# Optimization experiments

Measured on AMD Instinct MI355X. Metric: run time of the kernel, lower is better.

The kernel has to match this reference:

```python
import jax, jax.numpy as jnp
import numpy as np
import math

NHEADS = 4


def _mab(Q, K, qw, qb, kw, kb, vw, vb, ow, ob, mask):
    """MAB2 from tripletformer: multi-head attention (head split via cat(split,0)),
    softmax scale uses sqrt(FULL dim_V), masked_fill(mask==0, -1e10), residual on
    the projected Q, then O + relu(fc_o(O))."""
    dv = qw.shape[1]
    dh = dv // NHEADS
    B, Nq, _ = Q.shape
    Nk = K.shape[1]
    Qh = (Q @ qw + qb).reshape(B, Nq, NHEADS, dh).transpose(0, 2, 1, 3)  # B,h,Nq,dh
    Kh = (K @ kw + kb).reshape(B, Nk, NHEADS, dh).transpose(0, 2, 1, 3)
    Vh = (K @ vw + vb).reshape(B, Nk, NHEADS, dh).transpose(0, 2, 1, 3)
    att = jnp.einsum('bhqd,bhkd->bhqk', Qh, Kh) * (1.0 / math.sqrt(dv))
    att = jnp.where(mask, att, jnp.asarray(-1e10, att.dtype))
    A = jax.nn.softmax(att, axis=-1)
    Oh = Qh + jnp.einsum('bhqk,bhkd->bhqd', A, Vh)
    O = Oh.transpose(0, 2, 1, 3).reshape(B, Nq, dv)
    return O + jax.nn.relu(O @ ow + ob)


def _forward(context_x, value, mask, obs_len, iff_w, iff_b, ind_points,
             q0w, q0b, k0w, k0b, v0w, v0b, o0w, o0b,
             q1w, q1b, k1w, k1b, v1w, v1b, o1w, o1b):
    B, L = context_x.shape
    D = value.shape[-1]
    mflat = mask.reshape(B, L * D)
    # stable stream compaction: observed entries first, original (time-major,
    # channel-minor) order preserved; truncate to static obs_len
    order = jnp.argsort(-mflat, axis=-1, stable=True)[:, :obs_len]  # (B, N)
    T = jnp.broadcast_to(context_x[:, :, None], (B, L, D)).reshape(B, L * D)
    C = jnp.broadcast_to(jnp.arange(D, dtype=jnp.int32), (B, L, D)).reshape(B, L * D)
    U = value.reshape(B, L * D)
    take = lambda a: jnp.take_along_axis(a, order, axis=-1)
    T_, U_, mk_ = take(T), take(U), take(mflat)
    Ch = jax.nn.one_hot(take(C), D, dtype=value.dtype)  # one_hot(num_classes=dim-2)
    X = jnp.concatenate([Ch, T_[..., None], U_[..., None]], axis=-1) * mk_[..., None]
    Y = jax.nn.relu(X @ iff_w + iff_b) * mk_[..., None]
    key_valid = mk_ > 0                        # (B, N)
    mask1 = key_valid[:, None, None, :]        # mab0: mask padded keys
    mask2 = key_valid[:, None, :, None]        # mab1: mask padded query rows
    Z = Y
    n_layers = ind_points.shape[0]
    for i in range(n_layers):
        I = jnp.broadcast_to(ind_points[i], (B,) + ind_points[i].shape)
        H = _mab(I, Z, q0w[i], q0b[i], k0w[i], k0b[i], v0w[i], v0b[i], o0w[i], o0b[i], mask1)
        Zn = _mab(Z, H, q1w[i], q1b[i], k1w[i], k1b[i], v1w[i], v1b[i], o1w[i], o1b[i], mask2)
        Z = Zn * mk_[..., None] + Z
    return Z, mk_[..., None]


def setup_inputs() -> dict:
    B, L, D, OBS, DK, M, NL = 16, 512, 41, 4096, 128, 128, 3
    key = jax.random.key(0)
    ks = jax.random.split(key, 16)
    context_x = jnp.sort(jax.random.uniform(ks[0], (B, L), dtype=jnp.float32), axis=-1)
    value = jax.random.normal(ks[1], (B, L, D), dtype=jnp.float32)
    # exactly OBS observed entries per batch row -> static packed length
    r = jax.random.uniform(ks[2], (B, L * D))
    kth = jnp.sort(r, axis=-1)[:, OBS]
    mask = (r < kth[:, None]).astype(jnp.float32).reshape(B, L, D)

    def w(k, shape, fan):
        return jax.random.normal(k, shape, dtype=jnp.float32) / math.sqrt(fan)

    inp = dict(
        context_x=context_x, value=value, mask=mask, obs_len=OBS,
        iff_w=w(ks[3], (D + 2, DK), D + 2), iff_b=jnp.zeros((DK,), jnp.float32),
        ind_points=w(ks[4], (NL, M, DK), DK),
    )
    for j, n in enumerate(['q0', 'k0', 'v0', 'o0', 'q1', 'k1', 'v1', 'o1']):
        inp[n + 'w'] = w(ks[5 + j], (NL, DK, DK), DK)
        inp[n + 'b'] = jnp.zeros((NL, DK), jnp.float32)
    return inp


def reference(context_x, value, mask, obs_len, iff_w, iff_b, ind_points,
              q0w, q0b, k0w, k0b, v0w, v0b, o0w, o0b,
              q1w, q1b, k1w, k1b, v1w, v1b, o1w, o1b):
    return _forward(context_x, value, mask, obs_len, iff_w, iff_b, ind_points,
                    q0w, q0b, k0w, k0b, v0w, v0b, o0w, o0b,
                    q1w, q1b, k1w, k1b, v1w, v1b, o1w, o1b)
```

## Files before the change

### kernel.cpp

```cpp
#include <hip/hip_runtime.h>
#include <math.h>

#define NBATCH 16
#define SEQL   512
#define DIM    41
#define LDFLAT (SEQL*DIM)
#define OBS    4096
#define DK     128
#define NH     4
#define DH     32

typedef short bf16x8 __attribute__((ext_vector_type(8)));
typedef short short8v __attribute__((ext_vector_type(8)));
typedef float floatx4 __attribute__((ext_vector_type(4)));

__device__ __forceinline__ short f2bf(float f) {
  union { float f; unsigned u; } v;
  v.f = f;
  unsigned r = (v.u + 0x7fffu + ((v.u >> 16) & 1u)) >> 16;
  return (short)r;
}
__device__ __forceinline__ float bf2f(short s) {
  union { unsigned u; float f; } v;
  v.u = ((unsigned)(unsigned short)s) << 16;
  return v.f;
}

__device__ __forceinline__ void stage_w(short* Wl, const short* __restrict__ Wt,
                                        int tid) {
#pragma unroll
  for (int i = tid * 8; i < 128 * 128; i += 2048)
    *(int4*)&Wl[(i >> 7) * 136 + (i & 127)] = *(const int4*)&Wt[i];
}
__device__ __forceinline__ void load_af(const short* Xl, int wv, int lm,
                                        int quad, bf16x8 af[4]) {
#pragma unroll
  for (int kc = 0; kc < 4; kc++)
    af[kc] = *(bf16x8*)&Xl[(wv * 16 + lm) * 136 + kc * 32 + quad * 8];
}
__device__ __forceinline__ void gemm8(const short* Wl, const bf16x8 af[4],
                                      int lm, int quad, floatx4 acc[8]) {
#pragma unroll
  for (int nt = 0; nt < 8; nt++) acc[nt] = (floatx4){0.f, 0.f, 0.f, 0.f};
#pragma unroll
  for (int kc = 0; kc < 4; kc++) {
    bf16x8 a = af[kc];
#pragma unroll
    for (int nt = 0; nt < 8; nt++) {
      bf16x8 b = *(bf16x8*)&Wl[(nt * 16 + lm) * 136 + kc * 32 + quad * 8];
      acc[nt] = __builtin_amdgcn_mfma_f32_16x16x32_bf16(a, b, acc[nt], 0, 0, 0);
    }
  }
}
__device__ __forceinline__ void store_sl(short* Sl, const floatx4 acc[8],
                                         const float* __restrict__ bias,
                                         int wv, int lm, int quad) {
#pragma unroll
  for (int nt = 0; nt < 8; nt++) {
    int col = nt * 16 + lm;
    float bn = bias[col];
#pragma unroll
    for (int r = 0; r < 4; r++)
      Sl[(wv * 16 + quad * 4 + r) * 136 + col] = f2bf(acc[nt][r] + bn);
  }
}
__device__ __forceinline__ void write_hs(const short* Sl,
                                         short* __restrict__ out, int rb,
                                         int nshift, int tid) {
  int rr = tid >> 2, hh = tid & 3;
  int r = rb + rr;
  int bb = r >> nshift, nn = r & ((1 << nshift) - 1);
  size_t o = (((size_t)(bb * NH + hh) << nshift) + nn) * 32;
#pragma unroll
  for (int j = 0; j < 4; j++)
    *(int4*)&out[o + j * 8] = *(int4*)&Sl[rr * 136 + hh * 32 + j * 8];
}

__global__ __launch_bounds__(1024) void prep_build_kernel(
    const float* __restrict__ q0w, const float* __restrict__ k0w,
    const float* __restrict__ v0w, const float* __restrict__ o0w,
    const float* __restrict__ q1w, const float* __restrict__ k1w,
    const float* __restrict__ v1w, const float* __restrict__ o1w,
    short* __restrict__ Wt,
    const float* __restrict__ mask, int* __restrict__ order,
    float* __restrict__ mk_out, float* __restrict__ mk_out2) {
  __shared__ float Tl[128 * 132];
  __shared__ int wsums[16];
  __shared__ int s_total_ones;
  __shared__ int s_chunk_ones;
  __shared__ int s_ones_base;
  __shared__ int s_zeros_base;
  int tid = threadIdx.x;

  if (blockIdx.x < 24) {
    int id = blockIdx.x, l = id >> 3, wi = id & 7;
    const float* s;
    switch (wi) {
      case 0: s = q0w; break; case 1: s = k0w; break;
      case 2: s = v0w; break; case 3: s = o0w; break;
      case 4: s = q1w; break; case 5: s = k1w; break;
      case 6: s = v1w; break; default: s = o1w; break;
    }
    s += (size_t)l * 16384;
    for (int i = tid * 4; i < 16384; i += 4096) {
      int k = i >> 7, n = i & 127;
      float4 x = *(const float4*)&s[i];
      Tl[k * 132 + n + 0] = x.x; Tl[k * 132 + n + 1] = x.y;
      Tl[k * 132 + n + 2] = x.z; Tl[k * 132 + n + 3] = x.w;
    }
    __syncthreads();
    short* dst = Wt + (size_t)id * 16384;
    int n = tid >> 3, k0 = (tid & 7) * 16;
    for (int jc = 0; jc < 2; jc++) {
      short8v t;
#pragma unroll
      for (int j = 0; j < 8; j++) t[j] = f2bf(Tl[(k0 + jc * 8 + j) * 132 + n]);
      *(short8v*)&dst[n * 128 + k0 + jc * 8] = t;
    }
    return;
  }

  int b = blockIdx.x - 24;
  const float* m = mask + (size_t)b * LDFLAT;
  int lane = tid & 63, w = tid >> 6;

  int cnt = 0;
  for (int j = tid; j < LDFLAT; j += 1024) cnt += (m[j] > 0.f) ? 1 : 0;
  for (int off = 32; off > 0; off >>= 1) cnt += __shfl_xor(cnt, off);
  if (lane == 0) wsums[w] = cnt;
  __syncthreads();
  if (tid == 0) {
    int t = 0;
    for (int i = 0; i < 16; i++) t += wsums[i];
    s_total_ones = t; s_ones_base = 0; s_zeros_base = 0;
  }
  __syncthreads();
  int total_ones = s_total_ones;

  for (int c0 = 0; c0 < LDFLAT; c0 += 1024) {
    __syncthreads();
    int j = c0 + tid;
    bool valid = (j < LDFLAT);
    float mv = valid ? m[j] : 0.f;
    int one = (valid && mv > 0.f) ? 1 : 0;
    int v = one;
    for (int off = 1; off < 64; off <<= 1) {
      int t = __shfl_up(v, (unsigned)off);
      if (lane >= off) v += t;
    }
    if (lane == 63) wsums[w] = v;
    __syncthreads();
    if (tid == 0) {
      int run = 0;
      for (int i = 0; i < 16; i++) { int t = wsums[i]; wsums[i] = run; run += t; }
      s_chunk_ones = run;
    }
    __syncthreads();
    int ones_before = (v - one) + wsums[w];
    int ob = s_ones_base, zb = s_zeros_base, chunk_ones = s_chunk_ones;
    int rem = LDFLAT - c0;
    int chunk_valid = rem < 1024 ? rem : 1024;
    int valid_before = tid < rem ? tid : rem;
    if (valid) {
      int pos = one ? (ob + ones_before)
                    : (total_ones + zb + (valid_before - ones_before));
      if (pos < OBS) {
        order[b * OBS + pos] = j;
        mk_out[b * OBS + pos] = mv;
        mk_out2[b * OBS + pos] = mv;
      }
    }
    __syncthreads();
    if (tid == 0) {
      s_ones_base = ob + chunk_ones;
      s_zeros_base = zb + (chunk_valid - chunk_ones);
    }
  }
}

__global__ __launch_bounds__(256) void fusedA_kernel(
    const int* __restrict__ order, const float* __restrict__ mk_g,
    const float* __restrict__ cx, const float* __restrict__ value,
    const float* __restrict__ iff_w, const float* __restrict__ iff_b,
    float* __restrict__ Z,
    const short* __restrict__ Wk, const float* __restrict__ kbias,
    short* __restrict__ Kb,
    const short* __restrict__ Wv, const float* __restrict__ vbias,
    short* __restrict__ Vb,
    const short* __restrict__ Wq, const float* __restrict__ qbias,
    short* __restrict__ Qb,
    const float* __restrict__ indp, const short* __restrict__ WtAll,
    const float* __restrict__ q0b_all, short* __restrict__ qh_b) {
  __shared__ __align__(16) short Xl[64 * 136];
  __shared__ __align__(16) short Wl[128 * 136];
  __shared__ int   rdd[64];
  __shared__ float rdt[64], rdu[64], rdm[64];
  int tid = threadIdx.x;

  if (blockIdx.x >= 1024) {
    int id = blockIdx.x - 1024;
    int l = id >> 1, rbq = (id & 1) * 64;
    const float* X = indp + (size_t)l * 16384 + (size_t)rbq * 128;
    const short* W = WtAll + (size_t)(l * 8) * 16384;
    const float* bias = q0b_all + (size_t)l * 128;
    short* out = qh_b + (size_t)l * 16384;
    for (int i = tid * 4; i < 64 * 128; i += 1024) {
      int rr = i >> 7, c = i & 127;
      float4 x = *(const float4*)&X[i];
      *(short4*)&Xl[rr * 136 + c] =
          make_short4(f2bf(x.x), f2bf(x.y), f2bf(x.z), f2bf(x.w));
    }
    stage_w(Wl, W, tid);
    __syncthreads();
    int wv = tid >> 6, lane = tid & 63, lm = lane & 15, quad = lane >> 4;
    bf16x8 af[4];
    load_af(Xl, wv, lm, quad, af);
    floatx4 acc[8];
    gemm8(Wl, af, lm, quad, acc);
    __syncthreads();
    store_sl(Wl, acc, bias, wv, lm, quad);
    __syncthreads();
    write_hs(Wl, out, rbq, 7, tid);
    return;
  }

  int rb = blockIdx.x * 64;
  if (tid < 64) {
    int idx = rb + tid;
    int b = idx >> 12;
    int j = order[idx];
    int l = j / DIM;
    rdd[tid] = j - l * DIM;
    rdt[tid] = cx[b * SEQL + l];
    rdu[tid] = value[(size_t)b * LDFLAT + j];
    rdm[tid] = mk_g[idx];
  }
  stage_w(Wl, Wk, tid);
  __syncthreads();
  for (int i = tid; i < 64 * 128; i += 256) {
    int rr = i >> 7, k = i & 127;
    float y = iff_w[rdd[rr] * DK + k] + rdt[rr] * iff_w[41 * DK + k] +
              rdu[rr] * iff_w[42 * DK + k] + iff_b[k];
    float z = fmaxf(y, 0.f) * rdm[rr];
    Z[(size_t)(rb + rr) * DK + k] = z;
    Xl[rr * 136 + k] = f2bf(z);
  }
  __syncthreads();
  int wv = tid >> 6, lane = tid & 63, lm = lane & 15, quad = lane >> 4;
  bf16x8 af[4];
  load_af(Xl, wv, lm, quad, af);
  floatx4 acc[8];
  gemm8(Wl, af, lm, quad, acc);
  __syncthreads();
  store_sl(Wl, acc, kbias, wv, lm, quad);
  __syncthreads();
  write_hs(Wl, Kb, rb, 12, tid);
  __syncthreads();
  stage_w(Wl, Wv, tid);
  __syncthreads();
  gemm8(Wl, af, lm, quad, acc);
  __syncthreads();
  store_sl(Wl, acc, vbias, wv, lm, quad);
  __syncthreads();
  write_hs(Wl, Vb, rb, 12, tid);
  __syncthreads();
  stage_w(Wl, Wq, tid);
  __syncthreads();
  gemm8(Wl, af, lm, quad, acc);
  __syncthreads();
  store_sl(Wl, acc, qbias, wv, lm, quad);
  __syncthreads();
  write_hs(Wl, Qb, rb, 12, tid);
}

__global__ __launch_bounds__(256) void attn1_kernel(
    const short* __restrict__ Qh,
    const short* __restrict__ Kh, const short* __restrict__ Vh,
    const float* __restrict__ mk,
    float* __restrict__ Opart, float* __restrict__ mpart,
    float* __restrict__ lpart) {
  __shared__ __align__(16) short Ql[128 * 40];
  __shared__ __align__(16) short Kc[64 * 40];
  __shared__ __align__(16) short Vtc[32 * 72];
  __shared__ __align__(16) short Pl[128 * 72];
  __shared__ float mkc[64];
  int bh = blockIdx.x;
  int b = bh >> 2, h = bh & 3;
  int ks = blockIdx.y;
  int tid = threadIdx.x;
  int wv = tid >> 6, lane = tid & 63, lm = lane & 15, quad = lane >> 4;

  const short* qbg = Qh + (size_t)h * 128 * 32;
  for (int i = tid * 8; i < 128 * 32; i += 2048) {
    int r = i >> 5, c = i & 31;
    *(int4*)&Ql[r * 40 + c] = *(const int4*)&qbg[i];
  }
  __syncthreads();
  bf16x8 aq[2];
  aq[0] = *(bf16x8*)&Ql[(wv * 32 + lm) * 40 + quad * 8];
  aq[1] = *(bf16x8*)&Ql[(wv * 32 + 16 + lm) * 40 + quad * 8];

  float m_i[2][4], l_i[2][4];
  floatx4 oacc[2][2];
#pragma unroll
  for (int mt = 0; mt < 2; mt++) {
#pragma unroll
    for (int r = 0; r < 4; r++) { m_i[mt][r] = -1e30f; l_i[mt][r] = 0.f; }
    oacc[mt][0] = (floatx4){0.f, 0.f, 0.f, 0.f};
    oacc[mt][1] = (floatx4){0.f, 0.f, 0.f, 0.f};
  }
  const float scale = 0.08838834764831845f;
  const short* kbase = Kh + ((size_t)bh * OBS + ks * 512) * 32;
  const short* vbase = Vh + ((size_t)bh * OBS + ks * 512) * 32;
  const float* mkb = mk + (size_t)b * OBS + ks * 512;

  for (int ch = 0; ch < 8; ch++) {
    __syncthreads();
    {
      int i = tid * 8;
      int r = i >> 5, c = i & 31;
      *(int4*)&Kc[r * 40 + c] = *(const int4*)&kbase[ch * 2048 + i];
      int4 vv4 = *(const int4*)&vbase[ch * 2048 + i];
      short* vv = (short*)&vv4;
#pragma unroll
      for (int j = 0; j < 8; j++) Vtc[(c + j) * 72 + r] = vv[j];
    }
    if (tid < 64) mkc[tid] = mkb[ch * 64 + tid];
    __syncthreads();

    floatx4 sf[2][4];
#pragma unroll
    for (int nt = 0; nt < 4; nt++) {
      bf16x8 bfrag = *(bf16x8*)&Kc[(nt * 16 + lm) * 40 + quad * 8];
      floatx4 z = {0.f, 0.f, 0.f, 0.f};
      sf[0][nt] = __builtin_amdgcn_mfma_f32_16x16x32_bf16(aq[0], bfrag, z, 0, 0, 0);
      sf[1][nt] = __builtin_amdgcn_mfma_f32_16x16x32_bf16(aq[1], bfrag, z, 0, 0, 0);
    }
#pragma unroll
    for (int nt = 0; nt < 4; nt++) {
      float mkv = mkc[nt * 16 + lm];
      bool ok = mkv > 0.f;
#pragma unroll
      for (int mt = 0; mt < 2; mt++)
#pragma unroll
        for (int r = 0; r < 4; r++)
          sf[mt][nt][r] = ok ? sf[mt][nt][r] * scale : -1e10f;
    }
#pragma unroll
    for (int mt = 0; mt < 2; mt++) {
#pragma unroll
      for (int r = 0; r < 4; r++) {
        float mx = fmaxf(fmaxf(sf[mt][0][r], sf[mt][1][r]),
                         fmaxf(sf[mt][2][r], sf[mt][3][r]));
        mx = fmaxf(mx, __shfl_xor(mx, 1));
        mx = fmaxf(mx, __shfl_xor(mx, 2));
        mx = fmaxf(mx, __shfl_xor(mx, 4));
        mx = fmaxf(mx, __shfl_xor(mx, 8));
        float mn = fmaxf(m_i[mt][r], mx);
        float al = __expf(m_i[mt][r] - mn);
        float ps = 0.f;
#pragma unroll
        for (int nt = 0; nt < 4; nt++) {
          float p = __expf(sf[mt][nt][r] - mn);
          sf[mt][nt][r] = p;
          ps += p;
        }
        ps += __shfl_xor(ps, 1);
        ps += __shfl_xor(ps, 2);
        ps += __shfl_xor(ps, 4);
        ps += __shfl_xor(ps, 8);
        l_i[mt][r] = l_i[mt][r] * al + ps;
        m_i[mt][r] = mn;
        oacc[mt][0] *= al;
        oacc[mt][1] *= al;
      }
    }
#pragma unroll
    for (int mt = 0; mt < 2; mt++)
#pragma unroll
      for (int nt = 0; nt < 4; nt++)
#pragma unroll
        for (int r = 0; r < 4; r++)
          Pl[(wv * 32 + mt * 16 + quad * 4 + r) * 72 + nt * 16 + lm] =
              f2bf(sf[mt][nt][r]);
#pragma unroll
    for (int kc = 0; kc < 2; kc++) {
      bf16x8 vf0 = *(bf16x8*)&Vtc[lm * 72 + kc * 32 + quad * 8];
      bf16x8 vf1 = *(bf16x8*)&Vtc[(16 + lm) * 72 + kc * 32 + quad * 8];
#pragma unroll
      for (int mt = 0; mt < 2; mt++) {
        bf16x8 pf = *(bf16x8*)&Pl[(wv * 32 + mt * 16 + lm) * 72 + kc * 32 + quad * 8];
        oacc[mt][0] = __builtin_amdgcn_mfma_f32_16x16x32_bf16(pf, vf0, oacc[mt][0], 0, 0, 0);
        oacc[mt][1] = __builtin_amdgcn_mfma_f32_16x16x32_bf16(pf, vf1, oacc[mt][1], 0, 0, 0);
      }
    }
  }
  float* ob = Opart + (size_t)(ks * 64 + bh) * 128 * 32;
#pragma unroll
  for (int mt = 0; mt < 2; mt++) {
#pragma unroll
    for (int r = 0; r < 4; r++) {
      int row = wv * 32 + mt * 16 + quad * 4 + r;
      ob[(size_t)row * 32 + lm] = oacc[mt][0][r];
      ob[(size_t)row * 32 + 16 + lm] = oacc[mt][1][r];
      if (lm == 0) {
        mpart[(size_t)(ks * 64 + bh) * 128 + row] = m_i[mt][r];
        lpart[(size_t)(ks * 64 + bh) * 128 + row] = l_i[mt][r];
      }
    }
  }
}

__global__ __launch_bounds__(256) void fusedB_kernel(
    const float* __restrict__ Opart, const float* __restrict__ mpart,
    const float* __restrict__ lpart, const short* __restrict__ qh,
    const short* __restrict__ Wo, const float* __restrict__ obias,
    const short* __restrict__ Wk, const float* __restrict__ kbias,
    const short* __restrict__ Wv, const float* __restrict__ vbias,
    short* __restrict__ khb, short* __restrict__ vhb) {
  __shared__ __align__(16) short Xl[64 * 136];
  __shared__ __align__(16) short Wl[128 * 136];
  int tid = threadIdx.x;
  int rb = blockIdx.x * 64;
  int b = rb >> 7, n0 = rb & 127;
  {
    int rr = tid >> 2, hh = tid & 3;
    int n = n0 + rr;
    int bh = b * 4 + hh;
    float mv[8], lv[8], m = -1e30f;
#pragma unroll
    for (int s = 0; s < 8; s++) {
      mv[s] = mpart[(size_t)(s * 64 + bh) * 128 + n];
      lv[s] = lpart[(size_t)(s * 64 + bh) * 128 + n];
      m = fmaxf(m, mv[s]);
    }
    float l = 0.f;
    float oa[32];
#pragma unroll
    for (int d = 0; d < 32; d++) oa[d] = 0.f;
#pragma unroll
    for (int s = 0; s < 8; s++) {
      float w = __expf(mv[s] - m);
      l += lv[s] * w;
      const float* op = &Opart[((size_t)(s * 64 + bh) * 128 + n) * 32];
#pragma unroll
      for (int d4 = 0; d4 < 8; d4++) {
        float4 v = *(const float4*)&op[d4 * 4];
        oa[d4 * 4 + 0] += v.x * w; oa[d4 * 4 + 1] += v.y * w;
        oa[d4 * 4 + 2] += v.z * w; oa[d4 * 4 + 3] += v.w * w;
      }
    }
    float li = 1.f / l;
    const short* qp = &qh[((size_t)hh * 128 + n) * 32];
#pragma unroll
    for (int d = 0; d < 32; d++)
      Xl[rr * 136 + hh * 32 + d] = f2bf(bf2f(qp[d]) + oa[d] * li);
  }
  stage_w(Wl, Wo, tid);
  __syncthreads();
  int wv = tid >> 6, lane = tid & 63, lm = lane & 15, quad = lane >> 4;
  bf16x8 af[4];
  load_af(Xl, wv, lm, quad, af);
  floatx4 acc[8];
  gemm8(Wl, af, lm, quad, acc);
  __syncthreads();
#pragma unroll
  for (int nt = 0; nt < 8; nt++) {
    int col = nt * 16 + lm;
    float bn = obias[col];
#pragma unroll
    for (int r = 0; r < 4; r++) {
      int row = wv * 16 + quad * 4 + r;
      float ov = bf2f(Xl[row * 136 + col]);
      Wl[row * 136 + col] = f2bf(ov + fmaxf(acc[nt][r] + bn, 0.f));
    }
  }
  __syncthreads();
  for (int i = tid * 8; i < 64 * 128; i += 2048)
    *(int4*)&Xl[(i >> 7) * 136 + (i & 127)] = *(int4*)&Wl[(i >> 7) * 136 + (i & 127)];
  __syncthreads();
  load_af(Xl, wv, lm, quad, af);
  stage_w(Wl, Wk, tid);
  __syncthreads();
  gemm8(Wl, af, lm, quad, acc);
  __syncthreads();
  store_sl(Wl, acc, kbias, wv, lm, quad);
  __syncthreads();
  write_hs(Wl, khb, rb, 7, tid);
  __syncthreads();
  stage_w(Wl, Wv, tid);
  __syncthreads();
  gemm8(Wl, af, lm, quad, acc);
  __syncthreads();
  store_sl(Wl, acc, vbias, wv, lm, quad);
  __syncthreads();
  write_hs(Wl, vhb, rb, 7, tid);
}

__global__ __launch_bounds__(256) void attn2_kernel(
    const short* __restrict__ Qh, const short* __restrict__ Kh,
    const short* __restrict__ Vh, short* __restrict__ O) {
  __shared__ __align__(16) short Kl[128 * 40];
  __shared__ __align__(16) short Vt[32 * 136];
  __shared__ __align__(16) short Ql[64 * 40];
  __shared__ __align__(16) short Pl[64 * 136];
  int bh = blockIdx.x;
  int b = bh >> 2, h = bh & 3;
  int q0 = blockIdx.y * 64;
  int tid = threadIdx.x;
  int wv = tid >> 6, lane = tid & 63, lm = lane & 15, quad = lane >> 4;
  const short* kb = Kh + (size_t)bh * 128 * 32;
  const short* vb = Vh + (size_t)bh * 128 * 32;
  const short* qb = Qh + ((size_t)bh * OBS + q0) * 32;

  for (int i = tid * 8; i < 128 * 32; i += 2048) {
    int r = i >> 5, c = i & 31;
    *(int4*)&Kl[r * 40 + c] = *(const int4*)&kb[i];
  }
  for (int i = tid * 8; i < 64 * 32; i += 2048) {
    int r = i >> 5, c = i & 31;
    *(int4*)&Ql[r * 40 + c] = *(const int4*)&qb[i];
  }
  for (int i = tid * 8; i < 128 * 32; i += 2048) {
    int r = i >> 5, c = i & 31;
    int4 vv4 = *(const int4*)&vb[i];
    short* vv = (short*)&vv4;
#pragma unroll
    for (int j = 0; j < 8; j++) Vt[(c + j) * 136 + r] = vv[j];
  }
  __syncthreads();

  const float scale = 0.08838834764831845f;
  bf16x8 afrag = *(bf16x8*)&Ql[(wv * 16 + lm) * 40 + quad * 8];
  floatx4 sf[8];
#pragma unroll
  for (int nt = 0; nt < 8; nt++) {
    bf16x8 bfrag = *(bf16x8*)&Kl[(nt * 16 + lm) * 40 + quad * 8];
    floatx4 z = {0.f, 0.f, 0.f, 0.f};
    sf[nt] = __builtin_amdgcn_mfma_f32_16x16x32_bf16(afrag, bfrag, z, 0, 0, 0);
  }
#pragma unroll
  for (int nt = 0; nt < 8; nt++) sf[nt] *= scale;
  float linv[4];
#pragma unroll
  for (int r = 0; r < 4; r++) {
    float mx = sf[0][r];
#pragma unroll
    for (int nt = 1; nt < 8; nt++) mx = fmaxf(mx, sf[nt][r]);
    mx = fmaxf(mx, __shfl_xor(mx, 1));
    mx = fmaxf(mx, __shfl_xor(mx, 2));
    mx = fmaxf(mx, __shfl_xor(mx, 4));
    mx = fmaxf(mx, __shfl_xor(mx, 8));
    float sum = 0.f;
#pragma unroll
    for (int nt = 0; nt < 8; nt++) {
      float p = __expf(sf[nt][r] - mx);
      sf[nt][r] = p;
      sum += p;
    }
    sum += __shfl_xor(sum, 1);
    sum += __shfl_xor(sum, 2);
    sum += __shfl_xor(sum, 4);
    sum += __shfl_xor(sum, 8);
    linv[r] = 1.f / sum;
  }
#pragma unroll
  for (int nt = 0; nt < 8; nt++)
#pragma unroll
    for (int r = 0; r < 4; r++)
      Pl[(wv * 16 + quad * 4 + r) * 136 + nt * 16 + lm] = f2bf(sf[nt][r]);

  floatx4 oacc[2] = {{0.f, 0.f, 0.f, 0.f}, {0.f, 0.f, 0.f, 0.f}};
#pragma unroll
  for (int kc = 0; kc < 4; kc++) {
    bf16x8 pf = *(bf16x8*)&Pl[(wv * 16 + lm) * 136 + kc * 32 + quad * 8];
#pragma unroll
    for (int nt2 = 0; nt2 < 2; nt2++) {
      bf16x8 vf = *(bf16x8*)&Vt[(nt2 * 16 + lm) * 136 + kc * 32 + quad * 8];
      oacc[nt2] = __builtin_amdgcn_mfma_f32_16x16x32_bf16(pf, vf, oacc[nt2], 0, 0, 0);
    }
  }
  short* Ol = Pl;
#pragma unroll
  for (int nt2 = 0; nt2 < 2; nt2++) {
#pragma unroll
    for (int r = 0; r < 4; r++) {
      int qrow = wv * 16 + quad * 4 + r;
      float q = bf2f(Ql[qrow * 40 + nt2 * 16 + lm]);
      Ol[qrow * 136 + nt2 * 16 + lm] = f2bf(q + oacc[nt2][r] * linv[r]);
    }
  }
  int rr = tid >> 2, seg = tid & 3;
  size_t o = ((size_t)b * OBS + q0 + rr) * 128 + h * 32 + seg * 8;
  *(int4*)&O[o] = *(int4*)&Ol[rr * 136 + seg * 8];
}

__global__ __launch_bounds__(256) void fusedC_kernel(
    const short* __restrict__ Ob, const short* __restrict__ Wo,
    const float* __restrict__ obias, const float* __restrict__ mk,
    const float* __restrict__ Zin, float* __restrict__ Zout,
    const short* __restrict__ Wk, const float* __restrict__ kbias,
    short* __restrict__ Kb,
    const short* __restrict__ Wv, const float* __restrict__ vbias,
    short* __restrict__ Vb,
    const short* __restrict__ Wq, const float* __restrict__ qbias,
    short* __restrict__ Qb) {
  __shared__ __align__(16) short Xl[64 * 136];
  __shared__ __align__(16) short Wl[128 * 136];
  int tid = threadIdx.x;
  int rb = blockIdx.x * 64;
  for (int i = tid * 8; i < 64 * 128; i += 2048) {
    int rr = i >> 7, c = i & 127;
    *(int4*)&Xl[rr * 136 + c] = *(const int4*)&Ob[(size_t)(rb + rr) * 128 + c];
  }
  stage_w(Wl, Wo, tid);
  __syncthreads();
  int wv = tid >> 6, lane = tid & 63, lm = lane & 15, quad = lane >> 4;
  bf16x8 af[4];
  load_af(Xl, wv, lm, quad, af);
  floatx4 acc[8];
  gemm8(Wl, af, lm, quad, acc);
  __syncthreads();
  float* Fl = (float*)Wl;
#pragma unroll
  for (int nt = 0; nt < 8; nt++) {
    int col = nt * 16 + lm;
    float bn = obias[col];
#pragma unroll
    for (int r = 0; r < 4; r++) {
      int row = wv * 16 + quad * 4 + r;
      int gr = rb + row;
      float ov = bf2f(Xl[row * 136 + col]);
      float f = ov + fmaxf(acc[nt][r] + bn, 0.f);
      Fl[row * 132 + col] = Zin[(size_t)gr * 128 + col] + f * mk[gr];
    }
  }
  __syncthreads();
  {
    int rr = tid >> 2, seg = tid & 3;
    int gr = rb + rr;
#pragma unroll
    for (int j = 0; j < 8; j++) {
      float4 f = *(float4*)&Fl[rr * 132 + seg * 32 + j * 4];
      *(float4*)&Zout[(size_t)gr * 128 + seg * 32 + j * 4] = f;
      *(short4*)&Xl[rr * 136 + seg * 32 + j * 4] =
          make_short4(f2bf(f.x), f2bf(f.y), f2bf(f.z), f2bf(f.w));
    }
  }
  if (Wk == nullptr) return;
  __syncthreads();
  load_af(Xl, wv, lm, quad, af);
  stage_w(Wl, Wk, tid);
  __syncthreads();
  gemm8(Wl, af, lm, quad, acc);
  __syncthreads();
  store_sl(Wl, acc, kbias, wv, lm, quad);
  __syncthreads();
  write_hs(Wl, Kb, rb, 12, tid);
  __syncthreads();
  stage_w(Wl, Wv, tid);
  __syncthreads();
  gemm8(Wl, af, lm, quad, acc);
  __syncthreads();
  store_sl(Wl, acc, vbias, wv, lm, quad);
  __syncthreads();
  write_hs(Wl, Vb, rb, 12, tid);
  __syncthreads();
  stage_w(Wl, Wq, tid);
  __syncthreads();
  gemm8(Wl, af, lm, quad, acc);
  __syncthreads();
  store_sl(Wl, acc, qbias, wv, lm, quad);
  __syncthreads();
  write_hs(Wl, Qb, rb, 12, tid);
}

extern "C" void kernel_launch(void* const* d_in, const int* in_sizes, int n_in,
                              void* d_out, int out_size, void* d_ws,
                              size_t ws_size, hipStream_t stream) {
  const float* cx    = (const float*)d_in[0];
  const float* value = (const float*)d_in[1];
  const float* mask  = (const float*)d_in[2];
  const float* iff_w = (const float*)d_in[4];
  const float* iff_b = (const float*)d_in[5];
  const float* indp  = (const float*)d_in[6];
  const float* q0w = (const float*)d_in[7];  const float* q0b = (const float*)d_in[8];
  const float* k0w = (const float*)d_in[9];  const float* k0b = (const float*)d_in[10];
  const float* v0w = (const float*)d_in[11]; const float* v0b = (const float*)d_in[12];
  const float* o0w = (const float*)d_in[13]; const float* o0b = (const float*)d_in[14];
  const float* q1w = (const float*)d_in[15]; const float* q1b = (const float*)d_in[16];
  const float* k1w = (const float*)d_in[17]; const float* k1b = (const float*)d_in[18];
  const float* v1w = (const float*)d_in[19]; const float* v1b = (const float*)d_in[20];
  const float* o1w = (const float*)d_in[21]; const float* o1b = (const float*)d_in[22];

  char* ws = (char*)d_ws;
  short* Wt    = (short*)ws;  ws += (size_t)24 * 16384 * 2;
  int*   order = (int*)ws;    ws += (size_t)NBATCH * OBS * 4;
  float* mk_g  = (float*)ws;  ws += (size_t)NBATCH * OBS * 4;
  float* Z     = (float*)ws;  ws += (size_t)NBATCH * OBS * DK * 4;
  short* Qb    = (short*)ws;  ws += (size_t)NBATCH * OBS * DK * 2;
  short* Kb    = (short*)ws;  ws += (size_t)NBATCH * OBS * DK * 2;
  short* Vb    = (short*)ws;  ws += (size_t)NBATCH * OBS * DK * 2;
  short* Ob    = (short*)ws;  ws += (size_t)NBATCH * OBS * DK * 2;
  short* qh_b  = (short*)ws;  ws += (size_t)3 * 128 * DK * 2;
  short* khb   = (short*)ws;  ws += (size_t)NBATCH * NH * 128 * DH * 2;
  short* vhb   = (short*)ws;  ws += (size_t)NBATCH * NH * 128 * DH * 2;
  float* Opart = (float*)ws;  ws += (size_t)8 * 64 * 128 * 32 * 4;
  float* mpart = (float*)ws;  ws += (size_t)8 * 64 * 128 * 4;
  float* lpart = (float*)ws;  ws += (size_t)8 * 64 * 128 * 4;

  float* outZ  = (float*)d_out;
  float* outMk = outZ + (size_t)NBATCH * OBS * DK;

  prep_build_kernel<<<40, 1024, 0, stream>>>(q0w, k0w, v0w, o0w, q1w, k1w,
                                             v1w, o1w, Wt, mask, order, mk_g,
                                             outMk);

  const short* W[3][8];
  for (int l = 0; l < 3; l++)
    for (int wi = 0; wi < 8; wi++) W[l][wi] = Wt + (size_t)(l * 8 + wi) * 16384;

  fusedA_kernel<<<1030, 256, 0, stream>>>(
      order, mk_g, cx, value, iff_w, iff_b, Z,
      W[0][1], k0b, Kb, W[0][2], v0b, Vb, W[0][4], q1b, Qb,
      indp, Wt, q0b, qh_b);

  for (int l = 0; l < 3; l++) {
    attn1_kernel<<<dim3(64, 8), 256, 0, stream>>>(
        qh_b + (size_t)l * 16384, Kb, Vb, mk_g, Opart, mpart, lpart);
    fusedB_kernel<<<32, 256, 0, stream>>>(
        Opart, mpart, lpart, qh_b + (size_t)l * 16384,
        W[l][3], o0b + (size_t)l * 128,
        W[l][5], k1b + (size_t)l * 128,
        W[l][6], v1b + (size_t)l * 128, khb, vhb);
    attn2_kernel<<<dim3(64, 64), 256, 0, stream>>>(Qb, khb, vhb, Ob);
    if (l < 2) {
      fusedC_kernel<<<1024, 256, 0, stream>>>(
          Ob, W[l][7], o1b + (size_t)l * 128, mk_g, Z, Z,
          W[l + 1][1], k0b + (size_t)(l + 1) * 128, Kb,
          W[l + 1][2], v0b + (size_t)(l + 1) * 128, Vb,
          W[l + 1][4], q1b + (size_t)(l + 1) * 128, Qb);
    } else {
      fusedC_kernel<<<1024, 256, 0, stream>>>(
          Ob, W[l][7], o1b + (size_t)l * 128, mk_g, Z, outZ,
          nullptr, nullptr, nullptr, nullptr, nullptr, nullptr,
          nullptr, nullptr, nullptr);
    }
  }
}
```

Baseline: 518.4 us.

## Process 128 rows per block in projection kernels to reuse staged weights

```diff
diff --git a/kernel.cpp b/kernel.cpp
--- a/kernel.cpp
+++ b/kernel.cpp
@@ -74,6 +74,62 @@
 #pragma unroll
   for (int j = 0; j < 4; j++)
     *(int4*)&out[o + j * 8] = *(int4*)&Sl[rr * 136 + hh * 32 + j * 8];
+}
+__device__ __forceinline__ void gemm16(const short* Wl, const short* Xl,
+                                       int wv, int lm, int quad,
+                                       floatx4 acc[2][8]) {
+  bf16x8 af[2][4];
+#pragma unroll
+  for (int mt = 0; mt < 2; mt++)
+#pragma unroll
+    for (int kc = 0; kc < 4; kc++)
+      af[mt][kc] =
+          *(bf16x8*)&Xl[(wv * 32 + mt * 16 + lm) * 136 + kc * 32 + quad * 8];
+#pragma unroll
+  for (int mt = 0; mt < 2; mt++)
+#pragma unroll
+    for (int nt = 0; nt < 8; nt++) acc[mt][nt] = (floatx4){0.f, 0.f, 0.f, 0.f};
+#pragma unroll
+  for (int kc = 0; kc < 4; kc++) {
+#pragma unroll
+    for (int nt = 0; nt < 8; nt++) {
+      bf16x8 b = *(bf16x8*)&Wl[(nt * 16 + lm) * 136 + kc * 32 + quad * 8];
+      acc[0][nt] =
+          __builtin_amdgcn_mfma_f32_16x16x32_bf16(af[0][kc], b, acc[0][nt], 0, 0, 0);
+      acc[1][nt] =
+          __builtin_amdgcn_mfma_f32_16x16x32_bf16(af[1][kc], b, acc[1][nt], 0, 0, 0);
+    }
+  }
+}
+__device__ __forceinline__ void store_sl2(short* Sl, const floatx4 acc[2][8],
+                                          const float* __restrict__ bias,
+                                          int wv, int lm, int quad) {
+#pragma unroll
+  for (int mt = 0; mt < 2; mt++)
+#pragma unroll
+    for (int nt = 0; nt < 8; nt++) {
+      int col = nt * 16 + lm;
+      float bn = bias[col];
+#pragma unroll
+      for (int r = 0; r < 4; r++)
+        Sl[(wv * 32 + mt * 16 + quad * 4 + r) * 136 + col] =
+            f2bf(acc[mt][nt][r] + bn);
+    }
+}
+__device__ __forceinline__ void write_hs2(const short* Sl,
+                                          short* __restrict__ out, int rb,
+                                          int nshift, int tid) {
+  int rr = tid >> 1, half = tid & 1;
+  int r = rb + rr;
+  int bb = r >> nshift, nn = r & ((1 << nshift) - 1);
+#pragma unroll
+  for (int j2 = 0; j2 < 2; j2++) {
+    int hh = half * 2 + j2;
+    size_t o = (((size_t)(bb * NH + hh) << nshift) + nn) * 32;
+#pragma unroll
+    for (int j = 0; j < 4; j++)
+      *(int4*)&out[o + j * 8] = *(int4*)&Sl[rr * 136 + hh * 32 + j * 8];
+  }
 }
 
 __global__ __launch_bounds__(1024) void prep_build_kernel(
@@ -191,14 +247,15 @@
     short* __restrict__ Qb,
     const float* __restrict__ indp, const short* __restrict__ WtAll,
     const float* __restrict__ q0b_all, short* __restrict__ qh_b) {
-  __shared__ __align__(16) short Xl[64 * 136];
+  __shared__ __align__(16) short Xl[128 * 136];
   __shared__ __align__(16) short Wl[128 * 136];
-  __shared__ int   rdd[64];
-  __shared__ float rdt[64], rdu[64], rdm[64];
+  __shared__ int   rdd[128];
+  __shared__ float rdt[128], rdu[128], rdm[128];
   int tid = threadIdx.x;
-
-  if (blockIdx.x >= 1024) {
-    int id = blockIdx.x - 1024;
+  int wv = tid >> 6, lane = tid & 63, lm = lane & 15, quad = lane >> 4;
+
+  if (blockIdx.x >= 512) {
+    int id = blockIdx.x - 512;
     int l = id >> 1, rbq = (id & 1) * 64;
     const float* X = indp + (size_t)l * 16384 + (size_t)rbq * 128;
     const short* W = WtAll + (size_t)(l * 8) * 16384;
@@ -212,7 +269,6 @@
     }
     stage_w(Wl, W, tid);
     __syncthreads();
-    int wv = tid >> 6, lane = tid & 63, lm = lane & 15, quad = lane >> 4;
     bf16x8 af[4];
     load_af(Xl, wv, lm, quad, af);
     floatx4 acc[8];
@@ -224,8 +280,8 @@
     return;
   }
 
-  int rb = blockIdx.x * 64;
-  if (tid < 64) {
+  int rb = blockIdx.x * 128;
+  if (tid < 128) {
     int idx = rb + tid;
     int b = idx >> 12;
     int j = order[idx];
@@ -237,40 +293,42 @@
   }
   stage_w(Wl, Wk, tid);
   __syncthreads();
-  for (int i = tid; i < 64 * 128; i += 256) {
+  for (int i = tid * 4; i < 128 * 128; i += 1024) {
     int rr = i >> 7, k = i & 127;
-    float y = iff_w[rdd[rr] * DK + k] + rdt[rr] * iff_w[41 * DK + k] +
-              rdu[rr] * iff_w[42 * DK + k] + iff_b[k];
-    float z = fmaxf(y, 0.f) * rdm[rr];
-    Z[(size_t)(rb + rr) * DK + k] = z;
-    Xl[rr * 136 + k] = f2bf(z);
-  }
-  __syncthreads();
-  int wv = tid >> 6, lane = tid & 63, lm = lane & 15, quad = lane >> 4;
-  bf16x8 af[4];
-  load_af(Xl, wv, lm, quad, af);
-  floatx4 acc[8];
-  gemm8(Wl, af, lm, quad, acc);
-  __syncthreads();
-  store_sl(Wl, acc, kbias, wv, lm, quad);
-  __syncthreads();
-  write_hs(Wl, Kb, rb, 12, tid);
+    float4 w0 = *(const float4*)&iff_w[rdd[rr] * DK + k];
+    float4 w1 = *(const float4*)&iff_w[41 * DK + k];
+    float4 w2 = *(const float4*)&iff_w[42 * DK + k];
+    float4 b4 = *(const float4*)&iff_b[k];
+    float t = rdt[rr], u = rdu[rr], mkv = rdm[rr];
+    float4 z;
+    z.x = fmaxf(w0.x + t * w1.x + u * w2.x + b4.x, 0.f) * mkv;
+    z.y = fmaxf(w0.y + t * w1.y + u * w2.y + b4.y, 0.f) * mkv;
+    z.z = fmaxf(w0.z + t * w1.z + u * w2.z + b4.z, 0.f) * mkv;
+    z.w = fmaxf(w0.w + t * w1.w + u * w2.w + b4.w, 0.f) * mkv;
+    *(float4*)&Z[(size_t)(rb + rr) * DK + k] = z;
+    *(short4*)&Xl[rr * 136 + k] =
+        make_short4(f2bf(z.x), f2bf(z.y), f2bf(z.z), f2bf(z.w));
+  }
+  __syncthreads();
+  floatx4 acc[2][8];
+  gemm16(Wl, Xl, wv, lm, quad, acc);
+  __syncthreads();
+  store_sl2(Wl, acc, kbias, wv, lm, quad);
+  write_hs2(Wl, Kb, rb, 12, tid);
   __syncthreads();
   stage_w(Wl, Wv, tid);
   __syncthreads();
-  gemm8(Wl, af, lm, quad, acc);
-  __syncthreads();
-  store_sl(Wl, acc, vbias, wv, lm, quad);
-  __syncthreads();
-  write_hs(Wl, Vb, rb, 12, tid);
+  gemm16(Wl, Xl, wv, lm, quad, acc);
+  __syncthreads();
+  store_sl2(Wl, acc, vbias, wv, lm, quad);
+  write_hs2(Wl, Vb, rb, 12, tid);
   __syncthreads();
   stage_w(Wl, Wq, tid);
   __syncthreads();
-  gemm8(Wl, af, lm, quad, acc);
-  __syncthreads();
-  store_sl(Wl, acc, qbias, wv, lm, quad);
-  __syncthreads();
-  write_hs(Wl, Qb, rb, 12, tid);
+  gemm16(Wl, Xl, wv, lm, quad, acc);
+  __syncthreads();
+  store_sl2(Wl, acc, qbias, wv, lm, quad);
+  write_hs2(Wl, Qb, rb, 12, tid);
 }
 
 __global__ __launch_bounds__(256) void attn1_kernel(
@@ -605,74 +663,77 @@
     short* __restrict__ Vb,
     const short* __restrict__ Wq, const float* __restrict__ qbias,
     short* __restrict__ Qb) {
-  __shared__ __align__(16) short Xl[64 * 136];
+  __shared__ __align__(16) short Xl[128 * 136];
   __shared__ __align__(16) short Wl[128 * 136];
   int tid = threadIdx.x;
-  int rb = blockIdx.x * 64;
-  for (int i = tid * 8; i < 64 * 128; i += 2048) {
+  int rb = blockIdx.x * 128;
+  int wv = tid >> 6, lane = tid & 63, lm = lane & 15, quad = lane >> 4;
+  for (int i = tid * 8; i < 128 * 128; i += 2048) {
     int rr = i >> 7, c = i & 127;
     *(int4*)&Xl[rr * 136 + c] = *(const int4*)&Ob[(size_t)(rb + rr) * 128 + c];
   }
   stage_w(Wl, Wo, tid);
   __syncthreads();
-  int wv = tid >> 6, lane = tid & 63, lm = lane & 15, quad = lane >> 4;
-  bf16x8 af[4];
-  load_af(Xl, wv, lm, quad, af);
-  floatx4 acc[8];
-  gemm8(Wl, af, lm, quad, acc);
+  floatx4 acc[2][8];
+  gemm16(Wl, Xl, wv, lm, quad, acc);
   __syncthreads();
   float* Fl = (float*)Wl;
 #pragma unroll
-  for (int nt = 0; nt < 8; nt++) {
-    int col = nt * 16 + lm;
-    float bn = obias[col];
-#pragma unroll
-    for (int r = 0; r < 4; r++) {
-      int row = wv * 16 + quad * 4 + r;
-      int gr = rb + row;
-      float ov = bf2f(Xl[row * 136 + col]);
-      float f = ov + fmaxf(acc[nt][r] + bn, 0.f);
-      Fl[row * 132 + col] = Zin[(size_t)gr * 128 + col] + f * mk[gr];
-    }
-  }
-  __syncthreads();
-  {
-    int rr = tid >> 2, seg = tid & 3;
-    int gr = rb + rr;
-#pragma unroll
-    for (int j = 0; j < 8; j++) {
-      float4 f = *(float4*)&Fl[rr * 132 + seg * 32 + j * 4];
-      *(float4*)&Zout[(size_t)gr * 128 + seg * 32 + j * 4] = f;
-      *(short4*)&Xl[rr * 136 + seg * 32 + j * 4] =
-          make_short4(f2bf(f.x), f2bf(f.y), f2bf(f.z), f2bf(f.w));
+  for (int mt = 0; mt < 2; mt++) {
+    float mkv[4];
+#pragma unroll
+    for (int r = 0; r < 4; r++)
+      mkv[r] = mk[rb + wv * 32 + mt * 16 + quad * 4 + r];
+#pragma unroll
+    for (int nt = 0; nt < 8; nt++) {
+      int col = nt * 16 + lm;
+      float bn = obias[col];
+#pragma unroll
+      for (int r = 0; r < 4; r++) {
+        int lrow = wv * 16 + quad * 4 + r;
+        int xrow = wv * 32 + mt * 16 + quad * 4 + r;
+        int gr = rb + xrow;
+        float ov = bf2f(Xl[xrow * 136 + col]);
+        float f = ov + fmaxf(acc[mt][nt][r] + bn, 0.f);
+        Fl[lrow * 132 + col] = Zin[(size_t)gr * 128 + col] + f * mkv[r];
+      }
+    }
+    {
+      int rr = tid >> 2, seg = tid & 3;
+      int xrow = (rr >> 4) * 32 + mt * 16 + (rr & 15);
+      int gr = rb + xrow;
+#pragma unroll
+      for (int j = 0; j < 8; j++) {
+        float4 f = *(float4*)&Fl[rr * 132 + seg * 32 + j * 4];
+        *(float4*)&Zout[(size_t)gr * 128 + seg * 32 + j * 4] = f;
+        if (Wk)
+          *(short4*)&Xl[xrow * 136 + seg * 32 + j * 4] =
+              make_short4(f2bf(f.x), f2bf(f.y), f2bf(f.z), f2bf(f.w));
+      }
     }
   }
   if (Wk == nullptr) return;
   __syncthreads();
-  load_af(Xl, wv, lm, quad, af);
   stage_w(Wl, Wk, tid);
   __syncthreads();
-  gemm8(Wl, af, lm, quad, acc);
-  __syncthreads();
-  store_sl(Wl, acc, kbias, wv, lm, quad);
-  __syncthreads();
-  write_hs(Wl, Kb, rb, 12, tid);
+  gemm16(Wl, Xl, wv, lm, quad, acc);
+  __syncthreads();
+  store_sl2(Wl, acc, kbias, wv, lm, quad);
+  write_hs2(Wl, Kb, rb, 12, tid);
   __syncthreads();
   stage_w(Wl, Wv, tid);
   __syncthreads();
-  gemm8(Wl, af, lm, quad, acc);
-  __syncthreads();
-  store_sl(Wl, acc, vbias, wv, lm, quad);
-  __syncthreads();
-  write_hs(Wl, Vb, rb, 12, tid);
+  gemm16(Wl, Xl, wv, lm, quad, acc);
+  __syncthreads();
+  store_sl2(Wl, acc, vbias, wv, lm, quad);
+  write_hs2(Wl, Vb, rb, 12, tid);
   __syncthreads();
   stage_w(Wl, Wq, tid);
   __syncthreads();
-  gemm8(Wl, af, lm, quad, acc);
-  __syncthreads();
-  store_sl(Wl, acc, qbias, wv, lm, quad);
-  __syncthreads();
-  write_hs(Wl, Qb, rb, 12, tid);
+  gemm16(Wl, Xl, wv, lm, quad, acc);
+  __syncthreads();
+  store_sl2(Wl, acc, qbias, wv, lm, quad);
+  write_hs2(Wl, Qb, rb, 12, tid);
 }
 
 extern "C" void kernel_launch(void* const* d_in, const int* in_sizes, int n_in,
@@ -720,7 +781,7 @@
   for (int l = 0; l < 3; l++)
     for (int wi = 0; wi < 8; wi++) W[l][wi] = Wt + (size_t)(l * 8 + wi) * 16384;
 
-  fusedA_kernel<<<1030, 256, 0, stream>>>(
+  fusedA_kernel<<<518, 256, 0, stream>>>(
       order, mk_g, cx, value, iff_w, iff_b, Z,
       W[0][1], k0b, Kb, W[0][2], v0b, Vb, W[0][4], q1b, Qb,
       indp, Wt, q0b, qh_b);
@@ -735,13 +796,13 @@
         W[l][6], v1b + (size_t)l * 128, khb, vhb);
     attn2_kernel<<<dim3(64, 64), 256, 0, stream>>>(Qb, khb, vhb, Ob);
     if (l < 2) {
-      fusedC_kernel<<<1024, 256, 0, stream>>>(
+      fusedC_kernel<<<512, 256, 0, stream>>>(
           Ob, W[l][7], o1b + (size_t)l * 128, mk_g, Z, Z,
           W[l + 1][1], k0b + (size_t)(l + 1) * 128, Kb,
           W[l + 1][2], v0b + (size_t)(l + 1) * 128, Vb,
           W[l + 1][4], q1b + (size_t)(l + 1) * 128, Qb);
     } else {
-      fusedC_kernel<<<1024, 256, 0, stream>>>(
+      fusedC_kernel<<<512, 256, 0, stream>>>(
           Ob, W[l][7], o1b + (size_t)l * 128, mk_g, Z, outZ,
           nullptr, nullptr, nullptr, nullptr, nullptr, nullptr,
           nullptr, nullptr, nullptr);
```

Result: slower. 541.8 us (+4.5%).
